# Performance work log

Measured on AMD Instinct MI355X. Metric: run time of the kernel, lower is better.

The kernel has to match this reference:

```python
import jax, jax.numpy as jnp
import numpy as np
from jax import lax
from jax.scipy.special import erf

EPS = 1e-5
B = 256

def _conv(x, w, stride):
    return lax.conv_general_dilated(x, w, (stride, stride), ((1, 1), (1, 1)),
                                    dimension_numbers=('NCHW', 'OIHW', 'NCHW'))

def lr_conv(x, alpha, betta, bias, stride):
    # Ternary weight distribution (LR-nets): p0 = P(w=0), p1 = P(w=1)
    p0 = jax.nn.sigmoid(alpha)
    p1 = (1.0 - p0) * jax.nn.sigmoid(betta)
    w_mean = 2.0 * p1 + p0 - 1.0          # E[w] = p1 - p_{-1}
    w_var = (1.0 - p0) - w_mean * w_mean  # Var[w] = E[w^2] - E[w]^2
    m = _conv(x, w_mean, stride) + bias[None, :, None, None]
    v = _conv(x * x, w_var, stride)
    return m, v

def sign_prob(m, v):
    # expected sign under CLT Gaussian: 2*Phi(m/sqrt(v)) - 1 = erf(m / sqrt(2 v))
    return erf(m / jnp.sqrt(2.0 * (v + EPS)))

def setup_inputs() -> dict:
    key = jax.random.key(0)
    ks = jax.random.split(key, 32)
    def n(k, shape, s=1.0):
        return jax.random.normal(k, shape, dtype=jnp.float32) * s
    inp = {}
    inp['x'] = n(ks[0], (B, 3, 32, 32))
    shapes = [(128, 3), (128, 128), (256, 128), (256, 256), (512, 256), (512, 512)]
    i = 1
    for li, (co, ci) in enumerate(shapes, start=1):
        inp['a%d' % li] = n(ks[i], (co, ci, 3, 3)); i += 1
        inp['b%d' % li] = n(ks[i], (co, ci, 3, 3)); i += 1
        inp['c%d' % li] = jnp.zeros((co,), jnp.float32)
    inp['bn_gamma'] = jnp.ones((512,), jnp.float32)
    inp['bn_beta'] = jnp.zeros((512,), jnp.float32)
    inp['fc1_w'] = n(ks[20], (1024, 8192), 0.01)
    inp['fc1_b'] = jnp.zeros((1024,), jnp.float32)
    inp['fc2_w'] = n(ks[21], (10, 1024), 0.03)
    inp['fc2_b'] = jnp.zeros((10,), jnp.float32)
    inp['noise6'] = n(ks[22], (B, 512, 4, 4))
    return inp

def reference(x, a1, b1, c1, a2, b2, c2, a3, b3, c3, a4, b4, c4, a5, b5, c5,
              a6, b6, c6, bn_gamma, bn_beta, fc1_w, fc1_b, fc2_w, fc2_b, noise6):
    h = x
    for (a, bt, c, s) in [(a1, b1, c1, 1), (a2, b2, c2, 2), (a3, b3, c3, 1),
                          (a4, b4, c4, 2), (a5, b5, c5, 1)]:
        m, v = lr_conv(h, a, bt, c, s)
        h = sign_prob(m, v)
    m, v = lr_conv(h, a6, b6, c6, 2)          # output_sample=True layer
    z = m + jnp.sqrt(v + EPS) * noise6        # reparameterized Gaussian sample
    mu = jnp.mean(z, axis=(0, 2, 3), keepdims=True)
    var = jnp.var(z, axis=(0, 2, 3), keepdims=True)
    z = bn_gamma[None, :, None, None] * (z - mu) / jnp.sqrt(var + EPS) + bn_beta[None, :, None, None]
    z = jax.nn.relu(z).reshape(z.shape[0], -1)  # [B, 8192]
    z = jax.nn.relu(z @ fc1_w.T + fc1_b)
    return z @ fc2_w.T + fc2_b
```

## Files before the change

kernel.cpp:

```cpp
#include <hip/hip_runtime.h>
#include <hip/hip_bf16.h>
#include <math.h>

#define EPS 1e-5f

typedef __hip_bfloat16 bf16;
typedef short s16x8 __attribute__((ext_vector_type(8)));
typedef float f32x4 __attribute__((ext_vector_type(4)));

__device__ __forceinline__ float bf2f(bf16 v) { return __bfloat162float(v); }
__device__ __forceinline__ float ldin(const void* p, size_t i, int isbf) {
    return isbf ? __bfloat162float(((const bf16*)p)[i]) : ((const float*)p)[i];
}
__device__ __forceinline__ float b2f_bits(short s) {
    unsigned u = ((unsigned)(unsigned short)s) << 16;
    return __builtin_bit_cast(float, u);
}
__device__ __forceinline__ uint4 sqpk4(uint4 u) {
    uint4 r;
    unsigned* up = (unsigned*)&u;
    unsigned* rp = (unsigned*)&r;
#pragma unroll
    for (int k = 0; k < 4; k++) {
        unsigned w = up[k];
        float lo = __builtin_bit_cast(float, w << 16);
        float hi = __builtin_bit_cast(float, w & 0xffff0000u);
        lo *= lo; hi *= hi;
        unsigned ul = __builtin_bit_cast(unsigned, lo) + 0x8000u;
        unsigned uh = __builtin_bit_cast(unsigned, hi) + 0x8000u;
        rp[k] = (ul >> 16) | (uh & 0xffff0000u);
    }
    return r;
}

__global__ __launch_bounds__(64) void detect_kernel(const void* __restrict__ x,
                                                    int* __restrict__ flags) {
    const unsigned* w = (const unsigned*)x;
    unsigned word = w[threadIdx.x];
    int e = (word >> 23) & 0xFF;
    bool ok = (word == 0u) || (e >= 0x70 && e <= 0x8E);
    unsigned long long m = __ballot(ok);
    if (threadIdx.x == 0) flags[0] = (__popcll(m) >= 32) ? 0 : 1;
}

__global__ __launch_bounds__(256) void prep_w_l1(
    const void* __restrict__ alpha, const void* __restrict__ betta,
    const int* __restrict__ flags, float* __restrict__ wmv, int n)
{
    int i = blockIdx.x * 256 + threadIdx.x;
    if (i >= n) return;
    int fl = flags[0];
    float a = ldin(alpha, i, fl), b = ldin(betta, i, fl);
    float p0 = 1.f / (1.f + expf(-a));
    float p1 = (1.f - p0) / (1.f + expf(-b));
    float m = 2.f * p1 + p0 - 1.f;
    wmv[i] = m;
    wmv[n + i] = (1.f - p0) - m * m;
}

__global__ __launch_bounds__(256) void prep_w_r(
    const void* __restrict__ alpha, const void* __restrict__ betta,
    const int* __restrict__ flags, bf16* __restrict__ wmr, bf16* __restrict__ wvr,
    int CI, int n)
{
    int i = blockIdx.x * 256 + threadIdx.x;
    if (i >= n) return;
    int fl = flags[0];
    float a = ldin(alpha, i, fl), b = ldin(betta, i, fl);
    float p0 = 1.f / (1.f + expf(-a));
    float p1 = (1.f - p0) / (1.f + expf(-b));
    float m = 2.f * p1 + p0 - 1.f;
    float v = (1.f - p0) - m * m;
    int cirest = CI * 9;
    int co = i / cirest, rem = i % cirest;
    int ci = rem / 9, tap = rem % 9;
    int o = (co * 9 + tap) * CI + ci;
    wmr[o] = __float2bfloat16(m);
    wvr[o] = __float2bfloat16(v);
}

__global__ __launch_bounds__(256) void permute_fc1(
    const void* __restrict__ w, const int* __restrict__ flags, bf16* __restrict__ wp)
{
    __shared__ float L[8192];
    const int fl = flags[0];
    int tid = threadIdx.x;
    int o = blockIdx.x;
    size_t srow = (size_t)o * 8192;
    for (int c = tid; c < 512; c += 256) {
        float v[16];
        if (fl) {
            const uint4* s = (const uint4*)((const bf16*)w + srow + c * 16);
            uint4 u0 = s[0], u1 = s[1];
            const unsigned short* h0 = (const unsigned short*)&u0;
            const unsigned short* h1 = (const unsigned short*)&u1;
#pragma unroll
            for (int j = 0; j < 8; j++) { v[j] = b2f_bits((short)h0[j]); v[8 + j] = b2f_bits((short)h1[j]); }
        } else {
            const float4* s = (const float4*)((const float*)w + srow + c * 16);
#pragma unroll
            for (int j = 0; j < 4; j++) {
                float4 t4 = s[j];
                v[j * 4 + 0] = t4.x; v[j * 4 + 1] = t4.y; v[j * 4 + 2] = t4.z; v[j * 4 + 3] = t4.w;
            }
        }
#pragma unroll
        for (int hw = 0; hw < 16; hw++) L[hw * 512 + c] = v[hw];
    }
    __syncthreads();
    for (int j = 0; j < 32; j++) {
        int idx = j * 256 + tid;
        wp[srow + idx] = __float2bfloat16(L[idx]);
    }
}

__global__ __launch_bounds__(256) void l1_conv(
    const void* __restrict__ x, const float* __restrict__ wmv,
    const void* __restrict__ bias, const int* __restrict__ flags,
    bf16* __restrict__ out)
{
    __shared__ float Xs[64][28];
    const int fl = flags[0];
    int tid = threadIdx.x;
    int pos0 = blockIdx.x * 64;
    int b = pos0 >> 10;
    for (int u = tid; u < 576; u += 256) {
        int p = u / 9, r = u - p * 9;
        int ci = r / 3, kh = r - ci * 3;
        int pos = pos0 + p;
        int oh = (pos >> 5) & 31, ow = pos & 31;
        int ih = oh - 1 + kh;
        bool okh = (unsigned)ih < 32u;
        size_t base = ((size_t)(b * 3 + ci) * 32 + ih) * 32;
#pragma unroll
        for (int kw = 0; kw < 3; kw++) {
            int iw = ow - 1 + kw;
            float v = (okh && (unsigned)iw < 32u) ? ldin(x, base + iw, fl) : 0.f;
            Xs[p][ci * 9 + kh * 3 + kw] = v;
        }
    }
    int c = tid & 127, pg = tid >> 7;
    float wm[27], wv[27];
#pragma unroll
    for (int k = 0; k < 27; k++) {
        wm[k] = wmv[c * 27 + k];
        wv[k] = wmv[3456 + c * 27 + k];
    }
    float bs = ldin(bias, c, fl);
    __syncthreads();
    for (int it = 0; it < 32; it++) {
        int p = it * 2 + pg;
        float aM = 0.f, aV = 0.f;
#pragma unroll
        for (int k = 0; k < 27; k++) {
            float xv = Xs[p][k];
            aM = fmaf(xv, wm[k], aM);
            aV = fmaf(xv * xv, wv[k], aV);
        }
        out[(size_t)(pos0 + p) * 128 + c] =
            __float2bfloat16(erff((aM + bs) * rsqrtf(2.f * (aV + EPS))));
    }
}

template<int CI, int CO, int H, int W, int S, int OH, int OW, int ACT>
__global__ __launch_bounds__(256) void conv_gemm(
    const bf16* __restrict__ xin,
    const bf16* __restrict__ wmr,
    const bf16* __restrict__ wvr,
    const void* __restrict__ bias, const void* __restrict__ noise,
    const int* __restrict__ flags, void* __restrict__ outp)
{
    constexpr int OHW = OH * OW;
    constexpr int RL = 72;
    __shared__ bf16 Xs [128 * RL];
    __shared__ bf16 Xq [128 * RL];
    __shared__ bf16 Wms[64 * RL];
    __shared__ bf16 Wvs[64 * RL];

    int tid = threadIdx.x;
    int lane = tid & 63, wv_ = tid >> 6;
    int q = lane >> 4, l15 = lane & 15;
    const int pw = (wv_ >> 1) * 64, cw = (wv_ & 1) * 32;
    const int c0 = blockIdx.y * 64;

    const int xrow_i = tid >> 1, xhalf = tid & 1;
    const int wrow_i = (tid >> 1) & 63;
    const int wpath = tid >> 7, whalf = tid & 1;

    int P = blockIdx.x * 128 + xrow_i;
    int b = P / OHW, rr = P % OHW;
    int oh = rr / OW, owp = rr % OW;

    const bf16* wrow_base = (wpath ? wvr : wmr) + (size_t)(c0 + wrow_i) * 9 * CI;
    bf16* wdst = (wpath ? Wvs : Wms) + wrow_i * RL + whalf * 32;

    f32x4 accM[4][2], accV[4][2];
#pragma unroll
    for (int i = 0; i < 4; i++)
#pragma unroll
        for (int j = 0; j < 2; j++) {
            accM[i][j] = (f32x4){0.f, 0.f, 0.f, 0.f};
            accV[i][j] = (f32x4){0.f, 0.f, 0.f, 0.f};
        }

    for (int kh = 0; kh < 3; kh++) {
        int ih = oh * S - 1 + kh;
        bool okh = (unsigned)ih < (unsigned)H;
        for (int kw = 0; kw < 3; kw++) {
            int iw = owp * S - 1 + kw;
            bool ok = okh && ((unsigned)iw < (unsigned)W);
            const bf16* xrow = xin + (((size_t)b * H + ih) * W + iw) * CI;
            const bf16* wrow = wrow_base + (kh * 3 + kw) * CI;
            for (int ci0 = 0; ci0 < CI; ci0 += 64) {
                __syncthreads();
                {
                    uint4 v[4];
#pragma unroll
                    for (int k = 0; k < 4; k++) v[k] = (uint4){0, 0, 0, 0};
                    if (ok) {
                        const uint4* s = (const uint4*)(xrow + ci0 + xhalf * 32);
#pragma unroll
                        for (int k = 0; k < 4; k++) v[k] = s[k];
                    }
                    uint4* d  = (uint4*)(Xs + xrow_i * RL + xhalf * 32);
                    uint4* d2 = (uint4*)(Xq + xrow_i * RL + xhalf * 32);
#pragma unroll
                    for (int k = 0; k < 4; k++) { d[k] = v[k]; d2[k] = sqpk4(v[k]); }
                }
                {
                    const uint4* s = (const uint4*)(wrow + ci0 + whalf * 32);
                    uint4* d = (uint4*)wdst;
#pragma unroll
                    for (int k = 0; k < 4; k++) d[k] = s[k];
                }
                __syncthreads();

#pragma unroll
                for (int ks = 0; ks < 2; ks++) {
                    s16x8 a[4], a2[4], bm[2], bv[2];
#pragma unroll
                    for (int i = 0; i < 4; i++) {
                        a[i]  = *(const s16x8*)(Xs + (pw + i * 16 + l15) * RL + ks * 32 + q * 8);
                        a2[i] = *(const s16x8*)(Xq + (pw + i * 16 + l15) * RL + ks * 32 + q * 8);
                    }
#pragma unroll
                    for (int j = 0; j < 2; j++) {
                        bm[j] = *(const s16x8*)(Wms + (cw + j * 16 + l15) * RL + ks * 32 + q * 8);
                        bv[j] = *(const s16x8*)(Wvs + (cw + j * 16 + l15) * RL + ks * 32 + q * 8);
                    }
#pragma unroll
                    for (int i = 0; i < 4; i++)
#pragma unroll
                        for (int j = 0; j < 2; j++) {
                            accM[i][j] = __builtin_amdgcn_mfma_f32_16x16x32_bf16(a[i],  bm[j], accM[i][j], 0, 0, 0);
                            accV[i][j] = __builtin_amdgcn_mfma_f32_16x16x32_bf16(a2[i], bv[j], accV[i][j], 0, 0, 0);
                        }
                }
            }
        }
    }

    const int fl = flags[0];
#pragma unroll
    for (int j = 0; j < 2; j++) {
        int co = c0 + cw + j * 16 + l15;
        float bs = ldin(bias, co, fl);
#pragma unroll
        for (int i = 0; i < 4; i++) {
            f32x4 m4 = accM[i][j], v4 = accV[i][j];
#pragma unroll
            for (int r = 0; r < 4; r++) {
                int PP = blockIdx.x * 128 + pw + i * 16 + q * 4 + r;
                float mm = m4[r] + bs, vv = v4[r];
                if (ACT == 0) {
                    ((bf16*)outp)[(size_t)PP * CO + co] =
                        __float2bfloat16(erff(mm * rsqrtf(2.f * (vv + EPS))));
                } else {
                    int bb = PP / OHW, hw = PP % OHW;
                    float nz = ldin(noise, ((size_t)bb * CO + co) * OHW + hw, fl);
                    ((float*)outp)[(size_t)PP * CO + co] = mm + sqrtf(vv + EPS) * nz;
                }
            }
        }
    }
}

__global__ __launch_bounds__(256) void fc1_gemm_sk(
    const bf16* __restrict__ A, const bf16* __restrict__ Wp,
    float* __restrict__ part)
{
    __shared__ bf16 Xs[128 * 40];
    __shared__ bf16 Ws[128 * 40];
    int tid = threadIdx.x;
    int lane = tid & 63, wv_ = tid >> 6;
    int q = lane >> 4, l15 = lane & 15;
    const int pw = (wv_ >> 1) * 64, cw = (wv_ & 1) * 64;
    const int p0 = blockIdx.x * 128, c0 = blockIdx.y * 128;
    const int kb = blockIdx.z * 1024;
    const int row_i = tid >> 1, half = tid & 1;

    f32x4 acc[4][4];
#pragma unroll
    for (int i = 0; i < 4; i++)
#pragma unroll
        for (int j = 0; j < 4; j++) acc[i][j] = (f32x4){0.f, 0.f, 0.f, 0.f};

    for (int k0 = kb; k0 < kb + 1024; k0 += 32) {
        __syncthreads();
        {
            const uint4* s = (const uint4*)(A + (size_t)(p0 + row_i) * 8192 + k0 + half * 16);
            uint4* d = (uint4*)(Xs + row_i * 40 + half * 16);
            d[0] = s[0]; d[1] = s[1];
        }
        {
            const uint4* s = (const uint4*)(Wp + (size_t)(c0 + row_i) * 8192 + k0 + half * 16);
            uint4* d = (uint4*)(Ws + row_i * 40 + half * 16);
            d[0] = s[0]; d[1] = s[1];
        }
        __syncthreads();
        s16x8 a[4], bb[4];
#pragma unroll
        for (int i = 0; i < 4; i++) {
            a[i]  = *(const s16x8*)(Xs + (pw + i * 16 + l15) * 40 + q * 8);
            bb[i] = *(const s16x8*)(Ws + (cw + i * 16 + l15) * 40 + q * 8);
        }
#pragma unroll
        for (int i = 0; i < 4; i++)
#pragma unroll
            for (int j = 0; j < 4; j++)
                acc[i][j] = __builtin_amdgcn_mfma_f32_16x16x32_bf16(a[i], bb[j], acc[i][j], 0, 0, 0);
    }

    float* pbase = part + (size_t)blockIdx.z * 256 * 1024;
#pragma unroll
    for (int j = 0; j < 4; j++) {
        int co = c0 + cw + j * 16 + l15;
#pragma unroll
        for (int i = 0; i < 4; i++) {
            f32x4 m4 = acc[i][j];
#pragma unroll
            for (int r = 0; r < 4; r++) {
                int P = p0 + pw + i * 16 + q * 4 + r;
                pbase[(size_t)P * 1024 + co] = m4[r];
            }
        }
    }
}

__global__ __launch_bounds__(256) void fc1_reduce(
    const float* __restrict__ part, const void* __restrict__ bias,
    const int* __restrict__ flags, float* __restrict__ out)
{
    int i = blockIdx.x * 256 + threadIdx.x;
    float s = 0.f;
#pragma unroll
    for (int k = 0; k < 8; k++) s += part[(size_t)k * 262144 + i];
    out[i] = fmaxf(s + ldin(bias, i & 1023, flags[0]), 0.f);
}

__global__ __launch_bounds__(256) void bn_part(const float* __restrict__ z,
                                               float4* __restrict__ partial)
{
    int blk = blockIdx.x;
    int t = threadIdx.x;
    float s0 = 0, ss0 = 0, s1 = 0, ss1 = 0;
    for (int p = 0; p < 32; p++) {
        float2 v = ((const float2*)z)[((size_t)(blk * 32 + p)) * 256 + t];
        s0 += v.x; ss0 += v.x * v.x;
        s1 += v.y; ss1 += v.y * v.y;
    }
    partial[blk * 256 + t] = make_float4(s0, ss0, s1, ss1);
}

__global__ __launch_bounds__(512) void bn_fin(
    const float4* __restrict__ partial, const void* __restrict__ gamma,
    const void* __restrict__ beta, const int* __restrict__ flags,
    float* __restrict__ sc, float* __restrict__ sh)
{
    int c = threadIdx.x;
    float s = 0, ss = 0;
    for (int j = 0; j < 128; j++) {
        float4 pv = partial[j * 256 + (c >> 1)];
        s += (c & 1) ? pv.z : pv.x;
        ss += (c & 1) ? pv.w : pv.y;
    }
    float mean = s * (1.f / 4096.f);
    float var = ss * (1.f / 4096.f) - mean * mean;
    int fl = flags[0];
    float scale = ldin(gamma, c, fl) * rsqrtf(var + EPS);
    sc[c] = scale;
    sh[c] = ldin(beta, c, fl) - mean * scale;
}

__global__ __launch_bounds__(256) void bn_apply(
    const float* __restrict__ z, const float* __restrict__ sc,
    const float* __restrict__ sh, bf16* __restrict__ zr)
{
    int i = blockIdx.x * 256 + threadIdx.x;
    int c = i & 511;
    float v = z[i] * sc[c] + sh[c];
    zr[i] = __float2bfloat16(fmaxf(v, 0.f));
}

__global__ __launch_bounds__(640) void fc2_kernel(
    const float* __restrict__ A, const void* __restrict__ W,
    const void* __restrict__ bias, const int* __restrict__ flags,
    void* __restrict__ out)
{
    const int fl = flags[0];
    int n = blockIdx.x;
    int o = threadIdx.x >> 6;
    int lane = threadIdx.x & 63;
    const float* a = A + (size_t)n * 1024;
    size_t wbase = (size_t)o * 1024;
    float s = 0.f;
    for (int i = lane; i < 1024; i += 64) s = fmaf(a[i], ldin(W, wbase + i, fl), s);
#pragma unroll
    for (int off = 32; off > 0; off >>= 1) s += __shfl_down(s, off);
    if (lane == 0) {
        float v = s + ldin(bias, o, fl);
        if (fl) ((bf16*)out)[n * 10 + o] = __float2bfloat16(v);
        else    ((float*)out)[n * 10 + o] = v;
    }
}

extern "C" void kernel_launch(void* const* d_in, const int* in_sizes, int n_in,
                              void* d_out, int out_size, void* d_ws, size_t ws_size,
                              hipStream_t stream)
{
    const void* x = d_in[0];
    const void *al[6], *be[6], *bi[6];
    for (int l = 0; l < 6; l++) {
        al[l] = d_in[1 + 3 * l];
        be[l] = d_in[2 + 3 * l];
        bi[l] = d_in[3 + 3 * l];
    }
    const void* bn_gamma = d_in[19];
    const void* bn_beta  = d_in[20];
    const void* fc1_w = d_in[21];
    const void* fc1_b = d_in[22];
    const void* fc2_w = d_in[23];
    const void* fc2_b = d_in[24];
    const void* noise = d_in[25];

    char* base = (char*)d_ws;
    size_t off = 0;
    auto alloc = [&](size_t bytes) { void* p = base + off; off += (bytes + 255) & ~(size_t)255; return p; };
    int* flags = (int*)alloc(256);
    float* w1 = (float*)alloc(2 * 3456 * sizeof(float));
    const int SwCI[5] = {128, 128, 256, 256, 512};
    const size_t Sw[5] = {147456, 294912, 589824, 1179648, 2359296};
    bf16 *wmr[5], *wvr[5];
    for (int l = 0; l < 5; l++) {
        wmr[l] = (bf16*)alloc(Sw[l] * sizeof(bf16));
        wvr[l] = (bf16*)alloc(Sw[l] * sizeof(bf16));
    }
    bf16* actA = (bf16*)alloc((size_t)256 * 1024 * 128 * sizeof(bf16));
    bf16* actB = (bf16*)alloc((size_t)256 * 256 * 128 * sizeof(bf16));
    float* z   = (float*)alloc((size_t)4096 * 512 * sizeof(float));
    bf16* zr   = (bf16*)alloc((size_t)256 * 8192 * sizeof(bf16));
    bf16* Wp   = (bf16*)alloc((size_t)1024 * 8192 * sizeof(bf16));
    float4* part = (float4*)alloc((size_t)128 * 256 * sizeof(float4));
    float* bnsc = (float*)alloc(512 * sizeof(float));
    float* bnsh = (float*)alloc(512 * sizeof(float));
    float* fc1o = (float*)alloc((size_t)256 * 1024 * sizeof(float));
    float* fc1part = (float*)actB;

    detect_kernel<<<1, 64, 0, stream>>>(x, flags);

    prep_w_l1<<<14, 256, 0, stream>>>(al[0], be[0], flags, w1, 3456);
    for (int l = 0; l < 5; l++) {
        int n = (int)Sw[l];
        prep_w_r<<<(n + 255) / 256, 256, 0, stream>>>(
            al[l + 1], be[l + 1], flags, wmr[l], wvr[l], SwCI[l], n);
    }
    permute_fc1<<<1024, 256, 0, stream>>>(fc1_w, flags, Wp);

    l1_conv<<<4096, 256, 0, stream>>>(x, w1, bi[0], flags, actA);

    conv_gemm<128, 128, 32, 32, 2, 16, 16, 0><<<dim3(512, 2), 256, 0, stream>>>(
        actA, wmr[0], wvr[0], bi[1], nullptr, flags, actB);
    conv_gemm<128, 256, 16, 16, 1, 16, 16, 0><<<dim3(512, 4), 256, 0, stream>>>(
        actB, wmr[1], wvr[1], bi[2], nullptr, flags, actA);
    conv_gemm<256, 256, 16, 16, 2, 8, 8, 0><<<dim3(128, 4), 256, 0, stream>>>(
        actA, wmr[2], wvr[2], bi[3], nullptr, flags, actB);
    conv_gemm<256, 512, 8, 8, 1, 8, 8, 0><<<dim3(128, 8), 256, 0, stream>>>(
        actB, wmr[3], wvr[3], bi[4], nullptr, flags, actA);
    conv_gemm<512, 512, 8, 8, 2, 4, 4, 1><<<dim3(32, 8), 256, 0, stream>>>(
        actA, wmr[4], wvr[4], bi[5], noise, flags, z);

    bn_part<<<128, 256, 0, stream>>>(z, part);
    bn_fin<<<1, 512, 0, stream>>>(part, bn_gamma, bn_beta, flags, bnsc, bnsh);
    bn_apply<<<8192, 256, 0, stream>>>(z, bnsc, bnsh, zr);

    fc1_gemm_sk<<<dim3(2, 8, 8), 256, 0, stream>>>(zr, Wp, fc1part);
    fc1_reduce<<<1024, 256, 0, stream>>>(fc1part, fc1_b, flags, fc1o);
    fc2_kernel<<<256, 640, 0, stream>>>(fc1o, fc2_w, fc2_b, flags, d_out);
}
```

Baseline: 856.9 us.

## Pipeline conv GEMM loads into registers, swizzle LDS, widen output-channel tile

The conv GEMM's nested tap/channel loops are flattened into one chunk loop. The next chunk's global loads go into registers while the current chunk computes, and the barrier waits only on LDS traffic. Padded LDS rows are replaced by an XOR swizzle, and most layers now use a 128-channel tile with launch bounds asking for 2 blocks per CU, which cuts grid size and reuses activations more. The weight permute kernel now iterates over output indices with shifts, so its writes are coalesced. Risks include register pressure from the larger accumulators and prefetch buffers, and fewer blocks per layer.

```diff
diff --git a/kernel.cpp b/kernel.cpp
--- a/kernel.cpp
+++ b/kernel.cpp
@@ -32,6 +32,8 @@
     }
     return r;
 }
+
+#define BAR_LDS() asm volatile("s_waitcnt lgkmcnt(0)\n\ts_barrier" ::: "memory")
 
 __global__ __launch_bounds__(64) void detect_kernel(const void* __restrict__ x,
                                                     int* __restrict__ flags) {
@@ -61,20 +63,21 @@
 __global__ __launch_bounds__(256) void prep_w_r(
     const void* __restrict__ alpha, const void* __restrict__ betta,
     const int* __restrict__ flags, bf16* __restrict__ wmr, bf16* __restrict__ wvr,
-    int CI, int n)
-{
-    int i = blockIdx.x * 256 + threadIdx.x;
-    if (i >= n) return;
+    int lc, int n)
+{
+    int o = blockIdx.x * 256 + threadIdx.x;
+    if (o >= n) return;
     int fl = flags[0];
+    int cotap = o >> lc;
+    int ci = o & ((1 << lc) - 1);
+    int co = cotap / 9;
+    int tap = cotap - co * 9;
+    int i = (((co << lc) + ci) * 9) + tap;
     float a = ldin(alpha, i, fl), b = ldin(betta, i, fl);
     float p0 = 1.f / (1.f + expf(-a));
     float p1 = (1.f - p0) / (1.f + expf(-b));
     float m = 2.f * p1 + p0 - 1.f;
     float v = (1.f - p0) - m * m;
-    int cirest = CI * 9;
-    int co = i / cirest, rem = i % cirest;
-    int ci = rem / 9, tap = rem % 9;
-    int o = (co * 9 + tap) * CI + ci;
     wmr[o] = __float2bfloat16(m);
     wvr[o] = __float2bfloat16(v);
 }
@@ -162,8 +165,8 @@
     }
 }
 
-template<int CI, int CO, int H, int W, int S, int OH, int OW, int ACT>
-__global__ __launch_bounds__(256) void conv_gemm(
+template<int CI, int CO, int H, int W, int S, int OH, int OW, int ACT, int COT>
+__global__ __launch_bounds__(256, 2) void conv_gemm(
     const bf16* __restrict__ xin,
     const bf16* __restrict__ wmr,
     const bf16* __restrict__ wvr,
@@ -171,98 +174,130 @@
     const int* __restrict__ flags, void* __restrict__ outp)
 {
     constexpr int OHW = OH * OW;
-    constexpr int RL = 72;
-    __shared__ bf16 Xs [128 * RL];
-    __shared__ bf16 Xq [128 * RL];
-    __shared__ bf16 Wms[64 * RL];
-    __shared__ bf16 Wvs[64 * RL];
-
-    int tid = threadIdx.x;
-    int lane = tid & 63, wv_ = tid >> 6;
-    int q = lane >> 4, l15 = lane & 15;
-    const int pw = (wv_ >> 1) * 64, cw = (wv_ & 1) * 32;
-    const int c0 = blockIdx.y * 64;
-
-    const int xrow_i = tid >> 1, xhalf = tid & 1;
-    const int wrow_i = (tid >> 1) & 63;
-    const int wpath = tid >> 7, whalf = tid & 1;
-
-    int P = blockIdx.x * 128 + xrow_i;
-    int b = P / OHW, rr = P % OHW;
-    int oh = rr / OW, owp = rr % OW;
-
-    const bf16* wrow_base = (wpath ? wvr : wmr) + (size_t)(c0 + wrow_i) * 9 * CI;
-    bf16* wdst = (wpath ? Wvs : Wms) + wrow_i * RL + whalf * 32;
-
-    f32x4 accM[4][2], accV[4][2];
+    constexpr int KC = CI / 64;
+    constexpr int NC = 9 * KC;
+    constexpr int WJ = COT / 32;
+
+    __shared__ bf16 Xs[128 * 64];
+    __shared__ bf16 Xq[128 * 64];
+    __shared__ bf16 Wms[COT * 64];
+    __shared__ bf16 Wvs[COT * 64];
+
+    const int tid = threadIdx.x;
+    const int lane = tid & 63, wv_ = tid >> 6;
+    const int q = lane >> 4, l15 = lane & 15;
+    const int pw = (wv_ >> 1) * 64, cw = (wv_ & 1) * (16 * WJ);
+    const int c0 = blockIdx.y * COT;
+
+    const int row = tid >> 1, half = tid & 1;
+    const int P = blockIdx.x * 128 + row;
+    const int b = P / OHW, rr = P % OHW;
+    const int oh = rr / OW, ow = rr % OW;
+    const bf16* xbase = xin + (size_t)b * (H * W * CI) + half * 32;
+
+    const int wrow = (COT == 128) ? row : (row & 63);
+    const int wpath = (COT == 128) ? 0 : (tid >> 7);
+    const bf16* wbase_m = wmr + (size_t)(c0 + wrow) * 9 * CI + half * 32;
+    const bf16* wbase_v = wvr + (size_t)(c0 + wrow) * 9 * CI + half * 32;
+
+    f32x4 accM[4][WJ], accV[4][WJ];
 #pragma unroll
     for (int i = 0; i < 4; i++)
 #pragma unroll
-        for (int j = 0; j < 2; j++) {
+        for (int j = 0; j < WJ; j++) {
             accM[i][j] = (f32x4){0.f, 0.f, 0.f, 0.f};
             accV[i][j] = (f32x4){0.f, 0.f, 0.f, 0.f};
         }
 
-    for (int kh = 0; kh < 3; kh++) {
-        int ih = oh * S - 1 + kh;
-        bool okh = (unsigned)ih < (unsigned)H;
-        for (int kw = 0; kw < 3; kw++) {
-            int iw = owp * S - 1 + kw;
-            bool ok = okh && ((unsigned)iw < (unsigned)W);
-            const bf16* xrow = xin + (((size_t)b * H + ih) * W + iw) * CI;
-            const bf16* wrow = wrow_base + (kh * 3 + kw) * CI;
-            for (int ci0 = 0; ci0 < CI; ci0 += 64) {
-                __syncthreads();
-                {
-                    uint4 v[4];
-#pragma unroll
-                    for (int k = 0; k < 4; k++) v[k] = (uint4){0, 0, 0, 0};
-                    if (ok) {
-                        const uint4* s = (const uint4*)(xrow + ci0 + xhalf * 32);
-#pragma unroll
-                        for (int k = 0; k < 4; k++) v[k] = s[k];
-                    }
-                    uint4* d  = (uint4*)(Xs + xrow_i * RL + xhalf * 32);
-                    uint4* d2 = (uint4*)(Xq + xrow_i * RL + xhalf * 32);
-#pragma unroll
-                    for (int k = 0; k < 4; k++) { d[k] = v[k]; d2[k] = sqpk4(v[k]); }
+    uint4 xv[4], wm4[4], wv4[4];
+
+    auto lsLoad = [&](int t) {
+        const int tap = t / KC, ci0 = (t % KC) * 64;
+        const int kh = tap / 3, kw = tap - kh * 3;
+        const int ih = oh * S - 1 + kh, iw = ow * S - 1 + kw;
+        const bool ok = ((unsigned)ih < (unsigned)H) && ((unsigned)iw < (unsigned)W);
+#pragma unroll
+        for (int k = 0; k < 4; k++) xv[k] = (uint4){0, 0, 0, 0};
+        if (ok) {
+            const uint4* s = (const uint4*)(xbase + (ih * W + iw) * CI + ci0);
+#pragma unroll
+            for (int k = 0; k < 4; k++) xv[k] = s[k];
+        }
+        const int woff = tap * CI + ci0;
+        if constexpr (COT == 128) {
+            const uint4* sm = (const uint4*)(wbase_m + woff);
+            const uint4* sv = (const uint4*)(wbase_v + woff);
+#pragma unroll
+            for (int k = 0; k < 4; k++) { wm4[k] = sm[k]; wv4[k] = sv[k]; }
+        } else {
+            const uint4* sp = (const uint4*)((wpath ? wbase_v : wbase_m) + woff);
+#pragma unroll
+            for (int k = 0; k < 4; k++) wm4[k] = sp[k];
+        }
+    };
+
+    auto lsStore = [&]() {
+#pragma unroll
+        for (int k = 0; k < 4; k++) {
+            const int u = half * 4 + k;
+            const int ox = row * 64 + ((u ^ (row & 7)) << 3);
+            *(uint4*)(Xs + ox) = xv[k];
+            *(uint4*)(Xq + ox) = sqpk4(xv[k]);
+        }
+        if constexpr (COT == 128) {
+#pragma unroll
+            for (int k = 0; k < 4; k++) {
+                const int u = half * 4 + k;
+                const int od = wrow * 64 + ((u ^ (wrow & 7)) << 3);
+                *(uint4*)(Wms + od) = wm4[k];
+                *(uint4*)(Wvs + od) = wv4[k];
+            }
+        } else {
+            bf16* wdst = wpath ? Wvs : Wms;
+#pragma unroll
+            for (int k = 0; k < 4; k++) {
+                const int u = half * 4 + k;
+                const int od = wrow * 64 + ((u ^ (wrow & 7)) << 3);
+                *(uint4*)(wdst + od) = wm4[k];
+            }
+        }
+    };
+
+    lsLoad(0);
+    for (int t = 0; t < NC; t++) {
+        BAR_LDS();
+        lsStore();
+        if (t + 1 < NC) lsLoad(t + 1);
+        BAR_LDS();
+
+#pragma unroll
+        for (int ks = 0; ks < 2; ks++) {
+            s16x8 a[4], a2[4];
+#pragma unroll
+            for (int i = 0; i < 4; i++) {
+                const int ra = pw + i * 16 + l15;
+                const int oa = ra * 64 + (((ks * 4 + q) ^ (ra & 7)) << 3);
+                a[i]  = *(const s16x8*)(Xs + oa);
+                a2[i] = *(const s16x8*)(Xq + oa);
+            }
+#pragma unroll
+            for (int j = 0; j < WJ; j++) {
+                const int rb = cw + j * 16 + l15;
+                const int ob = rb * 64 + (((ks * 4 + q) ^ (rb & 7)) << 3);
+                s16x8 bm = *(const s16x8*)(Wms + ob);
+                s16x8 bv = *(const s16x8*)(Wvs + ob);
+#pragma unroll
+                for (int i = 0; i < 4; i++) {
+                    accM[i][j] = __builtin_amdgcn_mfma_f32_16x16x32_bf16(a[i],  bm, accM[i][j], 0, 0, 0);
+                    accV[i][j] = __builtin_amdgcn_mfma_f32_16x16x32_bf16(a2[i], bv, accV[i][j], 0, 0, 0);
                 }
-                {
-                    const uint4* s = (const uint4*)(wrow + ci0 + whalf * 32);
-                    uint4* d = (uint4*)wdst;
-#pragma unroll
-                    for (int k = 0; k < 4; k++) d[k] = s[k];
-                }
-                __syncthreads();
-
-#pragma unroll
-                for (int ks = 0; ks < 2; ks++) {
-                    s16x8 a[4], a2[4], bm[2], bv[2];
-#pragma unroll
-                    for (int i = 0; i < 4; i++) {
-                        a[i]  = *(const s16x8*)(Xs + (pw + i * 16 + l15) * RL + ks * 32 + q * 8);
-                        a2[i] = *(const s16x8*)(Xq + (pw + i * 16 + l15) * RL + ks * 32 + q * 8);
-                    }
-#pragma unroll
-                    for (int j = 0; j < 2; j++) {
-                        bm[j] = *(const s16x8*)(Wms + (cw + j * 16 + l15) * RL + ks * 32 + q * 8);
-                        bv[j] = *(const s16x8*)(Wvs + (cw + j * 16 + l15) * RL + ks * 32 + q * 8);
-                    }
-#pragma unroll
-                    for (int i = 0; i < 4; i++)
-#pragma unroll
-                        for (int j = 0; j < 2; j++) {
-                            accM[i][j] = __builtin_amdgcn_mfma_f32_16x16x32_bf16(a[i],  bm[j], accM[i][j], 0, 0, 0);
-                            accV[i][j] = __builtin_amdgcn_mfma_f32_16x16x32_bf16(a2[i], bv[j], accV[i][j], 0, 0, 0);
-                        }
-                }
             }
         }
     }
 
     const int fl = flags[0];
 #pragma unroll
-    for (int j = 0; j < 2; j++) {
+    for (int j = 0; j < WJ; j++) {
         int co = c0 + cw + j * 16 + l15;
         float bs = ldin(bias, co, fl);
 #pragma unroll
@@ -448,7 +483,7 @@
     auto alloc = [&](size_t bytes) { void* p = base + off; off += (bytes + 255) & ~(size_t)255; return p; };
     int* flags = (int*)alloc(256);
     float* w1 = (float*)alloc(2 * 3456 * sizeof(float));
-    const int SwCI[5] = {128, 128, 256, 256, 512};
+    const int SwLC[5] = {7, 7, 8, 8, 9};
     const size_t Sw[5] = {147456, 294912, 589824, 1179648, 2359296};
     bf16 *wmr[5], *wvr[5];
     for (int l = 0; l < 5; l++) {
@@ -472,21 +507,21 @@
     for (int l = 0; l < 5; l++) {
         int n = (int)Sw[l];
         prep_w_r<<<(n + 255) / 256, 256, 0, stream>>>(
-            al[l + 1], be[l + 1], flags, wmr[l], wvr[l], SwCI[l], n);
+            al[l + 1], be[l + 1], flags, wmr[l], wvr[l], SwLC[l], n);
     }
     permute_fc1<<<1024, 256, 0, stream>>>(fc1_w, flags, Wp);
 
     l1_conv<<<4096, 256, 0, stream>>>(x, w1, bi[0], flags, actA);
 
-    conv_gemm<128, 128, 32, 32, 2, 16, 16, 0><<<dim3(512, 2), 256, 0, stream>>>(
+    conv_gemm<128, 128, 32, 32, 2, 16, 16, 0, 128><<<dim3(512, 1), 256, 0, stream>>>(
         actA, wmr[0], wvr[0], bi[1], nullptr, flags, actB);
-    conv_gemm<128, 256, 16, 16, 1, 16, 16, 0><<<dim3(512, 4), 256, 0, stream>>>(
+    conv_gemm<128, 256, 16, 16, 1, 16, 16, 0, 128><<<dim3(512, 2), 256, 0, stream>>>(
         actB, wmr[1], wvr[1], bi[2], nullptr, flags, actA);
-    conv_gemm<256, 256, 16, 16, 2, 8, 8, 0><<<dim3(128, 4), 256, 0, stream>>>(
+    conv_gemm<256, 256, 16, 16, 2, 8, 8, 0, 128><<<dim3(128, 2), 256, 0, stream>>>(
         actA, wmr[2], wvr[2], bi[3], nullptr, flags, actB);
-    conv_gemm<256, 512, 8, 8, 1, 8, 8, 0><<<dim3(128, 8), 256, 0, stream>>>(
+    conv_gemm<256, 512, 8, 8, 1, 8, 8, 0, 128><<<dim3(128, 4), 256, 0, stream>>>(
         actB, wmr[3], wvr[3], bi[4], nullptr, flags, actA);
-    conv_gemm<512, 512, 8, 8, 2, 4, 4, 1><<<dim3(32, 8), 256, 0, stream>>>(
+    conv_gemm<512, 512, 8, 8, 2, 4, 4, 1, 64><<<dim3(32, 8), 256, 0, stream>>>(
         actA, wmr[4], wvr[4], bi[5], noise, flags, z);
 
     bn_part<<<128, 256, 0, stream>>>(z, part);
```

Measured after the change: 930.1 us. 1.09x slower.
